# Kernel tuning notes

Hardware: AMD Instinct MI355X
Metric: run time of the kernel (lower is better)

The kernel has to match this reference:

```python
import jax, jax.numpy as jnp
import numpy as np

B, S, H = 2, 4096, 1024
WINDOW = 32


def setup_inputs() -> dict:
    key = jax.random.key(0)
    ks = jax.random.split(key, 10)
    s = 1.0 / np.sqrt(H)
    return {
        "hidden_states": jax.random.normal(ks[0], (B, S, H), dtype=jnp.float32),
        "Wq": jax.random.normal(ks[1], (H, H), dtype=jnp.float32) * s,
        "Wk": jax.random.normal(ks[2], (H, H), dtype=jnp.float32) * s,
        "Wv": jax.random.normal(ks[3], (H, H), dtype=jnp.float32) * s,
        "Wo": jax.random.normal(ks[4], (H, H), dtype=jnp.float32) * s,
        "ln_w": jnp.ones((H,), dtype=jnp.float32),
        "ln_b": jnp.zeros((H,), dtype=jnp.float32),
        "W1": jax.random.normal(ks[5], (H // 2, H), dtype=jnp.float32) * s,
        "b1": jnp.zeros((H // 2,), dtype=jnp.float32),
        "W2": jax.random.normal(ks[6], (H, H // 2), dtype=jnp.float32) * (1.0 / np.sqrt(H // 2)),
        "b2": jnp.zeros((H,), dtype=jnp.float32),
    }


def _layernorm(x, w, b, eps=1e-5):
    mu = jnp.mean(x, axis=-1, keepdims=True)
    var = jnp.var(x, axis=-1, keepdims=True)
    return (x - mu) * jax.lax.rsqrt(var + eps) * w + b


def reference(hidden_states, Wq, Wk, Wv, Wo, ln_w, ln_b, W1, b1, W2, b2):
    x = hidden_states  # [B,S,H]
    q = x @ Wq.T
    k = x @ Wk.T
    v = x @ Wv.T
    # banded causal mask: keep j<=i and j >= i-WINDOW+1
    i = jnp.arange(S)[:, None]
    j = jnp.arange(S)[None, :]
    local_mask = (j <= i) & (j >= i - WINDOW + 1)  # [S,S] bool
    scores = jnp.einsum('bqh,bkh->bqk', q, k) / np.sqrt(H)
    scores = jnp.where(local_mask[None], scores, -jnp.inf)
    probs = jax.nn.softmax(scores, axis=-1)
    attn_out = jnp.einsum('bqk,bkh->bqh', probs, v) @ Wo.T
    draft = x + attn_out
    h = _layernorm(draft, ln_w, ln_b)
    h = jax.nn.gelu(h @ W1.T + b1, approximate=False)
    adapter_out = h @ W2.T + b2
    return draft + adapter_out
```

## Files before the change

### kernel.cpp

```cpp
#include <hip/hip_runtime.h>
#include <stdint.h>

typedef unsigned short u16;
typedef __bf16 bfx8 __attribute__((ext_vector_type(8)));
typedef float f32x4 __attribute__((ext_vector_type(4)));

__device__ __forceinline__ u16 f2bf(float x) {
    unsigned int u = __float_as_uint(x);
    u += 0x7fffu + ((u >> 16) & 1u);
    return (u16)(u >> 16);
}
__device__ __forceinline__ float bf2f(u16 v) {
    return __uint_as_float(((unsigned)v) << 16);
}

__device__ __forceinline__ void async16(const void* g, void* l) {
    __builtin_amdgcn_global_load_lds(
        (const __attribute__((address_space(1))) unsigned int*)(uintptr_t)g,
        (__attribute__((address_space(3))) unsigned int*)(unsigned int)(uintptr_t)l,
        16, 0, 0);
}

#define S_BARRIER() asm volatile("s_barrier" ::: "memory")
#define WAIT_VM6() asm volatile("s_waitcnt vmcnt(6)" ::: "memory")
#define WAIT_VM5() asm volatile("s_waitcnt vmcnt(5)" ::: "memory")
#define WAIT_VM0() asm volatile("s_waitcnt vmcnt(0)" ::: "memory")

struct CastArgs {
    const float* src[7];
    u16* dst[7];
    int nblk[7];
};
__global__ __launch_bounds__(256) void cast_all(CastArgs a) {
    int b = blockIdx.x, seg = 0;
    while (b >= a.nblk[seg]) { b -= a.nblk[seg]; ++seg; }
    int i = b * 256 + threadIdx.x;
    const float4* p = (const float4*)(a.src[seg] + (size_t)i * 8);
    float4 x = p[0], y = p[1];
    ushort4 o0, o1;
    o0.x = f2bf(x.x); o0.y = f2bf(x.y); o0.z = f2bf(x.z); o0.w = f2bf(x.w);
    o1.x = f2bf(y.x); o1.y = f2bf(y.y); o1.z = f2bf(y.z); o1.w = f2bf(y.w);
    ushort4* q = (ushort4*)(a.dst[seg] + (size_t)i * 8);
    q[0] = o0; q[1] = o1;
}

template <int EPI, int BNv>
__global__ __launch_bounds__(512, 2)
void gemm_ring(const u16* __restrict__ A, const u16* __restrict__ Bw,
               u16* __restrict__ outq, u16* __restrict__ outk,
               u16* __restrict__ vt, u16* __restrict__ outb,
               const float* __restrict__ bias, const u16* __restrict__ resb,
               u16* __restrict__ draftb, float* __restrict__ outf,
               int M, int N, int K, int ncol) {
    constexpr int NF = BNv / 32;
    constexpr int BU = BNv / 64;
    constexpr int TS = 32768 + BNv * 128;
    __shared__ __align__(1024) unsigned char lds[3 * TS];
    const int t = threadIdx.x;
    const int lane = t & 63, w = t >> 6;
    const int laneR = lane & 15, laneK = lane >> 4;
    const int wr = w >> 1, wc = w & 1;
    const int b = blockIdx.x;
    const int cpx = gridDim.x >> 3;
    const int swz = (b & 7) * cpx + (b >> 3);
    const int row0 = (swz / ncol) * 256, col0 = (swz % ncol) * BNv;
    const int nt = K >> 6;

    f32x4 acc[4][NF] = {};

    const u16* srcA[4];
    const u16* srcB[BU];
    unsigned dA[4], dB[BU];
#pragma unroll
    for (int i = 0; i < 4; ++i) {
        int li = i * 512 + t;
        int row = li >> 3, ko = li & 7;
        srcA[i] = A + (size_t)(row0 + row) * K + (ko ^ (row & 7)) * 8;
        dA[i] = li * 16;
    }
#pragma unroll
    for (int i = 0; i < BU; ++i) {
        int li = i * 512 + t;
        int row = li >> 3, ko = li & 7;
        srcB[i] = Bw + (size_t)(col0 + row) * K + (ko ^ (row & 7)) * 8;
        dB[i] = 32768 + li * 16;
    }

    auto stage = [&](int rb, int tk, int h) {
        unsigned char* base = lds + rb * TS;
        const int o = tk * 64;
        if (h == 0) {
            async16(srcA[0] + o, base + dA[0]);
            async16(srcA[1] + o, base + dA[1]);
            async16(srcB[0] + o, base + dB[0]);
        } else {
            async16(srcA[2] + o, base + dA[2]);
            async16(srcA[3] + o, base + dA[3]);
            if constexpr (BU == 2) async16(srcB[1] + o, base + dB[1]);
        }
    };

    stage(0, 0, 0); stage(0, 0, 1);
    stage(1, 1, 0); stage(1, 1, 1);

    for (int tk = 0; tk < nt; ++tk) {
        unsigned char* bufA = lds + (tk % 3) * TS;
        unsigned char* bufB = bufA + 32768;
        if (tk + 1 < nt) {
            if constexpr (BU == 2) { WAIT_VM6(); } else { WAIT_VM5(); }
        } else { WAIT_VM0(); }
        S_BARRIER();
        const bool pf = (tk + 2 < nt);
        const int nb = (tk + 2) % 3;
#pragma unroll
        for (int ks = 0; ks < 2; ++ks) {
            bfx8 af[4], bf[NF];
#pragma unroll
            for (int m = 0; m < 4; ++m) {
                int r = wr * 64 + m * 16 + laneR;
                int phys = (ks * 4 + laneK) ^ (r & 7);
                af[m] = *(const bfx8*)(bufA + r * 128 + phys * 16);
            }
#pragma unroll
            for (int n = 0; n < NF; ++n) {
                int r = wc * (BNv / 2) + n * 16 + laneR;
                int phys = (ks * 4 + laneK) ^ (r & 7);
                bf[n] = *(const bfx8*)(bufB + r * 128 + phys * 16);
            }
            if (pf) stage(nb, tk + 2, ks);
            S_BARRIER();
            __builtin_amdgcn_s_setprio(1);
#pragma unroll
            for (int m = 0; m < 4; ++m)
#pragma unroll
                for (int n = 0; n < NF; ++n)
                    acc[m][n] = __builtin_amdgcn_mfma_f32_16x16x32_bf16(
                        af[m], bf[n], acc[m][n], 0, 0, 0);
            __builtin_amdgcn_s_setprio(0);
            S_BARRIER();
        }
    }

#pragma unroll
    for (int m = 0; m < 4; ++m) {
        const int gr0 = row0 + wr * 64 + m * 16 + laneK * 4;
#pragma unroll
        for (int n = 0; n < NF; ++n) {
            const int gc = col0 + wc * (BNv / 2) + n * 16 + laneR;
            if constexpr (EPI == 0) {
                if (col0 < 1024) {
#pragma unroll
                    for (int r = 0; r < 4; ++r)
                        outq[(size_t)(gr0 + r) * 1024 + gc] = f2bf(acc[m][n][r]);
                } else if (col0 < 2048) {
#pragma unroll
                    for (int r = 0; r < 4; ++r)
                        outk[(size_t)(gr0 + r) * 1024 + (gc - 1024)] = f2bf(acc[m][n][r]);
                } else {
                    ushort4 o4;
                    o4.x = f2bf(acc[m][n][0]); o4.y = f2bf(acc[m][n][1]);
                    o4.z = f2bf(acc[m][n][2]); o4.w = f2bf(acc[m][n][3]);
                    *(ushort4*)(vt + (((size_t)(gr0 >> 12)) * 1024 + (gc - 2048)) * 4096 +
                                (gr0 & 4095)) = o4;
                }
            } else if constexpr (EPI == 1) {
#pragma unroll
                for (int r = 0; r < 4; ++r) {
                    size_t idx = (size_t)(gr0 + r) * N + gc;
                    draftb[idx] = f2bf(bf2f(resb[idx]) + acc[m][n][r]);
                }
            } else if constexpr (EPI == 2) {
#pragma unroll
                for (int r = 0; r < 4; ++r) {
                    float xx = acc[m][n][r] + bias[gc];
                    outb[(size_t)(gr0 + r) * N + gc] =
                        f2bf(xx * 0.5f * (1.0f + erff(xx * 0.70710678118654752f)));
                }
            } else {
#pragma unroll
                for (int r = 0; r < 4; ++r) {
                    size_t idx = (size_t)(gr0 + r) * N + gc;
                    outf[idx] = bf2f(draftb[idx]) + acc[m][n][r] + bias[gc];
                }
            }
        }
    }
}

__global__ __launch_bounds__(256, 2)
void attn_kernel(const u16* __restrict__ Q, const u16* __restrict__ K,
                 const u16* __restrict__ vt, u16* __restrict__ O) {
    constexpr int H = 1024, S = 4096;
    const int t = threadIdx.x, lane = t & 63, w = t >> 6;
    const int laneR = lane & 15, laneK = lane >> 4;
    const int bb = blockIdx.x;
    const int tile = (bb & 7) * 32 + (bb >> 3);
    const int batch = tile >> 7;
    const int i0 = (tile & 127) * 32;
    const size_t base = (size_t)batch * S * H;

    __shared__ __align__(16) float S4[4][32][64];
    __shared__ __align__(16) u16 P[32][72];

    f32x4 sc[2][4] = {};
    for (int h = w * 256; h < w * 256 + 256; h += 32) {
        bfx8 qa[2];
#pragma unroll
        for (int m = 0; m < 2; ++m) {
            size_t row = (size_t)(i0 + m * 16 + laneR);
            qa[m] = *(const bfx8*)(Q + base + row * H + h + laneK * 8);
        }
        bfx8 kb[4];
#pragma unroll
        for (int n = 0; n < 4; ++n) {
            int j = i0 - 32 + n * 16 + laneR;
            int jc = j < 0 ? 0 : j;
            kb[n] = *(const bfx8*)(K + base + (size_t)jc * H + h + laneK * 8);
        }
#pragma unroll
        for (int m = 0; m < 2; ++m)
#pragma unroll
            for (int n = 0; n < 4; ++n)
                sc[m][n] = __builtin_amdgcn_mfma_f32_16x16x32_bf16(
                    qa[m], kb[n], sc[m][n], 0, 0, 0);
    }
#pragma unroll
    for (int m = 0; m < 2; ++m)
#pragma unroll
        for (int n = 0; n < 4; ++n)
#pragma unroll
            for (int r = 0; r < 4; ++r)
                S4[w][m * 16 + laneK * 4 + r][n * 16 + laneR] = sc[m][n][r];
    __syncthreads();

    {
        int q = t >> 3;
        int c0 = (t & 7) * 8;
        int lo = q + 1;
        if (32 - i0 > lo) lo = 32 - i0;
        int hi = q + 32;
        float vals[8];
        float mx = -1e30f;
#pragma unroll
        for (int c = 0; c < 8; ++c) {
            int cc = c0 + c;
            float v = (S4[0][q][cc] + S4[1][q][cc] + S4[2][q][cc] + S4[3][q][cc]) * 0.03125f;
            bool valid = (cc >= lo) && (cc <= hi);
            vals[c] = valid ? v : -1e30f;
            if (vals[c] > mx) mx = vals[c];
        }
#pragma unroll
        for (int d = 1; d < 8; d <<= 1) {
            float o = __shfl_xor(mx, d);
            if (o > mx) mx = o;
        }
        float sum = 0.f;
        float es[8];
#pragma unroll
        for (int c = 0; c < 8; ++c) {
            es[c] = (vals[c] > -1e29f) ? __expf(vals[c] - mx) : 0.f;
            sum += es[c];
        }
#pragma unroll
        for (int d = 1; d < 8; d <<= 1) sum += __shfl_xor(sum, d);
        float inv = 1.0f / sum;
#pragma unroll
        for (int c = 0; c < 8; ++c) P[q][c0 + c] = f2bf(es[c] * inv);
    }
    __syncthreads();

    for (int nc = 0; nc < 4; ++nc) {
        int ncol = w * 256 + nc * 64;
        f32x4 o[2][4] = {};
#pragma unroll
        for (int ks = 0; ks < 2; ++ks) {
            bfx8 pa[2];
#pragma unroll
            for (int m = 0; m < 2; ++m)
                pa[m] = *(const bfx8*)(&P[m * 16 + laneR][ks * 32 + laneK * 8]);
            int t0 = i0 - 32 + ks * 32 + laneK * 8;
            if (t0 < 0) t0 = 0;
#pragma unroll
            for (int n = 0; n < 4; ++n) {
                int c = ncol + n * 16 + laneR;
                bfx8 vb = *(const bfx8*)(vt + ((size_t)batch * 1024 + c) * 4096 + t0);
#pragma unroll
                for (int m = 0; m < 2; ++m)
                    o[m][n] = __builtin_amdgcn_mfma_f32_16x16x32_bf16(
                        pa[m], vb, o[m][n], 0, 0, 0);
            }
        }
#pragma unroll
        for (int m = 0; m < 2; ++m)
#pragma unroll
            for (int n = 0; n < 4; ++n)
#pragma unroll
                for (int r = 0; r < 4; ++r) {
                    size_t row = (size_t)(i0 + m * 16 + laneK * 4 + r);
                    O[base + row * H + ncol + n * 16 + laneR] = f2bf(o[m][n][r]);
                }
    }
}

__global__ __launch_bounds__(256)
void ln_kernel(const u16* __restrict__ xb, const float* __restrict__ gw,
               const float* __restrict__ gb, u16* __restrict__ out) {
    const int row = blockIdx.x, t = threadIdx.x;
    const ushort4 dv = ((const ushort4*)(xb + (size_t)row * 1024))[t];
    float4 v;
    v.x = bf2f(dv.x); v.y = bf2f(dv.y); v.z = bf2f(dv.z); v.w = bf2f(dv.w);
    float s = v.x + v.y + v.z + v.w;
    float s2 = v.x * v.x + v.y * v.y + v.z * v.z + v.w * v.w;
#pragma unroll
    for (int d = 1; d < 64; d <<= 1) {
        s += __shfl_xor(s, d);
        s2 += __shfl_xor(s2, d);
    }
    __shared__ float red[8];
    int lane = t & 63, wv = t >> 6;
    if (lane == 0) { red[wv] = s; red[4 + wv] = s2; }
    __syncthreads();
    float S1 = red[0] + red[1] + red[2] + red[3];
    float S2 = red[4] + red[5] + red[6] + red[7];
    float mu = S1 * (1.0f / 1024.0f);
    float var = S2 * (1.0f / 1024.0f) - mu * mu;
    float rstd = rsqrtf(var + 1e-5f);
    const float4 wv4 = ((const float4*)gw)[t];
    const float4 bv4 = ((const float4*)gb)[t];
    ushort4 o;
    o.x = f2bf((v.x - mu) * rstd * wv4.x + bv4.x);
    o.y = f2bf((v.y - mu) * rstd * wv4.y + bv4.y);
    o.z = f2bf((v.z - mu) * rstd * wv4.z + bv4.z);
    o.w = f2bf((v.w - mu) * rstd * wv4.w + bv4.w);
    ((ushort4*)(out + (size_t)row * 1024))[t] = o;
}

extern "C" void kernel_launch(void* const* d_in, const int* in_sizes, int n_in,
                              void* d_out, int out_size, void* d_ws, size_t ws_size,
                              hipStream_t stream) {
    const float* x   = (const float*)d_in[0];
    const float* Wq  = (const float*)d_in[1];
    const float* Wk  = (const float*)d_in[2];
    const float* Wv  = (const float*)d_in[3];
    const float* Wo  = (const float*)d_in[4];
    const float* lnw = (const float*)d_in[5];
    const float* lnb = (const float*)d_in[6];
    const float* W1  = (const float*)d_in[7];
    const float* b1  = (const float*)d_in[8];
    const float* W2  = (const float*)d_in[9];
    const float* b2  = (const float*)d_in[10];
    (void)in_sizes; (void)n_in; (void)out_size; (void)ws_size;

    const int M = 8192, H = 1024, Hh = 512;

    char* ws = (char*)d_ws;
    size_t off = 0;
    auto alloc = [&](size_t bytes) {
        char* p = ws + off;
        off += (bytes + 255) & ~(size_t)255;
        return p;
    };
    u16* Xb     = (u16*)alloc((size_t)M * H * 2);
    u16* Wqkvb  = (u16*)alloc((size_t)3 * H * H * 2);
    u16* Wob    = (u16*)alloc((size_t)H * H * 2);
    u16* W1b    = (u16*)alloc((size_t)Hh * H * 2);
    u16* W2b    = (u16*)alloc((size_t)H * Hh * 2);
    u16* Qb     = (u16*)alloc((size_t)M * H * 2);
    u16* Kb     = (u16*)alloc((size_t)M * H * 2);
    u16* Vt     = (u16*)alloc((size_t)M * H * 2);
    u16* draftb = (u16*)alloc((size_t)M * H * 2);
    u16* Attb   = (u16*)alloc((size_t)M * H * 2);
    u16* hlnb = Qb;
    u16* Gb   = Kb;
    float* outp = (float*)d_out;

    CastArgs ca;
    ca.src[0] = x;  ca.dst[0] = Xb;                        ca.nblk[0] = (M * H / 8) / 256;
    ca.src[1] = Wq; ca.dst[1] = Wqkvb;                     ca.nblk[1] = (H * H / 8) / 256;
    ca.src[2] = Wk; ca.dst[2] = Wqkvb + (size_t)H * H;     ca.nblk[2] = (H * H / 8) / 256;
    ca.src[3] = Wv; ca.dst[3] = Wqkvb + (size_t)2 * H * H; ca.nblk[3] = (H * H / 8) / 256;
    ca.src[4] = Wo; ca.dst[4] = Wob;                       ca.nblk[4] = (H * H / 8) / 256;
    ca.src[5] = W1; ca.dst[5] = W1b;                       ca.nblk[5] = (Hh * H / 8) / 256;
    ca.src[6] = W2; ca.dst[6] = W2b;                       ca.nblk[6] = (H * Hh / 8) / 256;
    int totblk = 0;
    for (int i = 0; i < 7; ++i) totblk += ca.nblk[i];
    cast_all<<<dim3(totblk), dim3(256), 0, stream>>>(ca);

    gemm_ring<0, 128><<<dim3(768), dim3(512), 0, stream>>>(
        Xb, Wqkvb, Qb, Kb, Vt, nullptr, nullptr, nullptr, nullptr, nullptr,
        M, 3 * H, H, 24);

    attn_kernel<<<dim3(256), dim3(256), 0, stream>>>(Qb, Kb, Vt, Attb);

    gemm_ring<1, 128><<<dim3(256), dim3(512), 0, stream>>>(
        Attb, Wob, nullptr, nullptr, nullptr, nullptr, nullptr, Xb, draftb, nullptr,
        M, H, H, 8);

    ln_kernel<<<dim3(M), dim3(256), 0, stream>>>(draftb, lnw, lnb, hlnb);

    gemm_ring<2, 64><<<dim3(256), dim3(512), 0, stream>>>(
        hlnb, W1b, nullptr, nullptr, nullptr, Gb, b1, nullptr, nullptr, nullptr,
        M, Hh, H, 8);

    gemm_ring<3, 128><<<dim3(256), dim3(512), 0, stream>>>(
        Gb, W2b, nullptr, nullptr, nullptr, nullptr, b2, nullptr, draftb, outp,
        M, H, Hh, 8);
}
```

Before: 168.8 us.

## Add dedicated 256x256-tile QKV GEMM with double-buffered staged loads

Replaces the generic 256x128 ring GEMM for the fused QKV projection with a specialised kernel using 256x256 tiles, a 2x4 wave layout and 128 KB double-buffered LDS. Loads for the next k-tile are interleaved in quarter-chunks between MFMA phases. This is meant to raise operand reuse and cut global traffic per FLOP. The generic GEMM also moves its vmcnt wait and barrier to the end of each iteration so the wait overlaps the tail of the MFMA phase. Risks include lower occupancy from the large LDS footprint, more barriers per iteration, and fewer blocks (384) to fill the GPU.

New measurement: 167.9 us. Within noise of the previous version (-0.5%).

```diff
diff --git a/kernel.cpp b/kernel.cpp
--- a/kernel.cpp
+++ b/kernel.cpp
@@ -24,6 +24,7 @@
 #define S_BARRIER() asm volatile("s_barrier" ::: "memory")
 #define WAIT_VM6() asm volatile("s_waitcnt vmcnt(6)" ::: "memory")
 #define WAIT_VM5() asm volatile("s_waitcnt vmcnt(5)" ::: "memory")
+#define WAIT_VM2() asm volatile("s_waitcnt vmcnt(2)" ::: "memory")
 #define WAIT_VM0() asm volatile("s_waitcnt vmcnt(0)" ::: "memory")
 
 struct CastArgs {
@@ -44,14 +45,149 @@
     q[0] = o0; q[1] = o1;
 }
 
+__global__ __launch_bounds__(512, 2)
+void gemm_qkv2(const u16* __restrict__ A, const u16* __restrict__ Bw,
+               u16* __restrict__ outq, u16* __restrict__ outk,
+               u16* __restrict__ vt, int K) {
+    __shared__ __align__(1024) unsigned char lds[131072];
+    const int t = threadIdx.x;
+    const int lane = t & 63, w = t >> 6;
+    const int laneR = lane & 15, laneK = lane >> 4;
+    const int wm = w >> 2, wn = w & 3;
+    const int b = blockIdx.x;
+    const int swz = (b & 7) * 48 + (b >> 3);
+    const int row0 = (swz / 12) * 256;
+    const int col0 = (swz % 12) * 256;
+    const int nt = K >> 6;
+
+    const u16* srcU[4][2];
+    unsigned dstU[4][2];
+#pragma unroll
+    for (int u = 0; u < 4; ++u)
+#pragma unroll
+        for (int j = 0; j < 2; ++j) {
+            int c = ((u & 1) ? 1024 : 0) + j * 512 + t;
+            int row = c >> 3;
+            int ko = (c & 7) ^ (row & 7);
+            if (u < 2) srcU[u][j] = A + (size_t)(row0 + row) * K + ko * 8;
+            else       srcU[u][j] = Bw + (size_t)(col0 + row) * K + ko * 8;
+            dstU[u][j] = (u >= 2 ? 32768u : 0u) + (unsigned)c * 16u;
+        }
+
+#define QSTAGE(U, D, TK)                                                      \
+    async16(srcU[U][0] + (TK) * 64, lds + (D) + dstU[U][0]);                  \
+    async16(srcU[U][1] + (TK) * 64, lds + (D) + dstU[U][1]);
+
+    f32x4 acc[8][4] = {};
+    bfx8 af[4], bf[4];
+
+#define QLDA(D, KS, H)                                                        \
+    _Pragma("unroll") for (int m = 0; m < 4; ++m) {                           \
+        int r = (H) * 128 + wm * 64 + m * 16 + laneR;                         \
+        int ph = ((KS) * 4 + laneK) ^ (r & 7);                                \
+        af[m] = *(const bfx8*)(lds + (D) + r * 128 + ph * 16);                \
+    }
+#define QLDB(D, KS)                                                           \
+    _Pragma("unroll") for (int n = 0; n < 4; ++n) {                           \
+        int rb = wn * 64 + n * 16 + laneR;                                    \
+        int ph = ((KS) * 4 + laneK) ^ (rb & 7);                               \
+        bf[n] = *(const bfx8*)(lds + (D) + 32768u + rb * 128 + ph * 16);      \
+    }
+#define QMFMA(H)                                                              \
+    __builtin_amdgcn_s_setprio(1);                                            \
+    _Pragma("unroll") for (int m = 0; m < 4; ++m)                             \
+        _Pragma("unroll") for (int n = 0; n < 4; ++n)                         \
+            acc[(H) * 4 + m][n] = __builtin_amdgcn_mfma_f32_16x16x32_bf16(    \
+                af[m], bf[n], acc[(H) * 4 + m][n], 0, 0, 0);                  \
+    __builtin_amdgcn_s_setprio(0);
+
+    QSTAGE(0, 0u, 0) QSTAGE(2, 0u, 0) QSTAGE(3, 0u, 0) QSTAGE(1, 0u, 0)
+    WAIT_VM2();
+    S_BARRIER();
+
+    for (int tk = 0; tk < nt - 1; ++tk) {
+        const unsigned d = (unsigned)(tk & 1) * 65536u;
+        const unsigned nd = d ^ 65536u;
+        const int tn = tk + 1;
+        QLDA(d, 0, 0) QLDB(d, 0) QSTAGE(0, nd, tn)
+        S_BARRIER();
+        QMFMA(0)
+        WAIT_VM2();
+        S_BARRIER();
+        QLDA(d, 0, 1) QSTAGE(2, nd, tn)
+        S_BARRIER();
+        QMFMA(1)
+        S_BARRIER();
+        QLDA(d, 1, 0) QLDB(d, 1) QSTAGE(3, nd, tn)
+        S_BARRIER();
+        QMFMA(0)
+        S_BARRIER();
+        QLDA(d, 1, 1) QSTAGE(1, nd, tn)
+        S_BARRIER();
+        QMFMA(1)
+        WAIT_VM2();
+        S_BARRIER();
+    }
+    {
+        const unsigned d = (unsigned)((nt - 1) & 1) * 65536u;
+        QLDA(d, 0, 0) QLDB(d, 0)
+        S_BARRIER();
+        QMFMA(0)
+        WAIT_VM0();
+        S_BARRIER();
+        QLDA(d, 0, 1)
+        S_BARRIER();
+        QMFMA(1)
+        S_BARRIER();
+        QLDA(d, 1, 0) QLDB(d, 1)
+        S_BARRIER();
+        QMFMA(0)
+        S_BARRIER();
+        QLDA(d, 1, 1)
+        S_BARRIER();
+        QMFMA(1)
+    }
+
+    const int colsec = col0 >> 10;
+#pragma unroll
+    for (int hi = 0; hi < 2; ++hi) {
+#pragma unroll
+        for (int mi = 0; mi < 4; ++mi) {
+            const int gr0 = row0 + hi * 128 + wm * 64 + mi * 16 + laneK * 4;
+#pragma unroll
+            for (int n = 0; n < 4; ++n) {
+                const int gc = col0 + wn * 64 + n * 16 + laneR;
+                const f32x4 a4 = acc[hi * 4 + mi][n];
+                if (colsec == 0) {
+#pragma unroll
+                    for (int r = 0; r < 4; ++r)
+                        outq[(size_t)(gr0 + r) * 1024 + gc] = f2bf(a4[r]);
+                } else if (colsec == 1) {
+#pragma unroll
+                    for (int r = 0; r < 4; ++r)
+                        outk[(size_t)(gr0 + r) * 1024 + (gc - 1024)] = f2bf(a4[r]);
+                } else {
+                    ushort4 o4;
+                    o4.x = f2bf(a4[0]); o4.y = f2bf(a4[1]);
+                    o4.z = f2bf(a4[2]); o4.w = f2bf(a4[3]);
+                    *(ushort4*)(vt + (((size_t)(gr0 >> 12)) * 1024 + (gc - 2048)) * 4096 +
+                                (gr0 & 4095)) = o4;
+                }
+            }
+        }
+    }
+#undef QSTAGE
+#undef QLDA
+#undef QLDB
+#undef QMFMA
+}
+
 template <int EPI, int BNv>
 __global__ __launch_bounds__(512, 2)
 void gemm_ring(const u16* __restrict__ A, const u16* __restrict__ Bw,
-               u16* __restrict__ outq, u16* __restrict__ outk,
-               u16* __restrict__ vt, u16* __restrict__ outb,
-               const float* __restrict__ bias, const u16* __restrict__ resb,
-               u16* __restrict__ draftb, float* __restrict__ outf,
-               int M, int N, int K, int ncol) {
+               u16* __restrict__ outb, const float* __restrict__ bias,
+               const u16* __restrict__ resb, u16* __restrict__ draftb,
+               float* __restrict__ outf, int M, int N, int K, int ncol) {
     constexpr int NF = BNv / 32;
     constexpr int BU = BNv / 64;
     constexpr int TS = 32768 + BNv * 128;
@@ -102,14 +238,12 @@
 
     stage(0, 0, 0); stage(0, 0, 1);
     stage(1, 1, 0); stage(1, 1, 1);
+    if constexpr (BU == 2) { WAIT_VM6(); } else { WAIT_VM5(); }
+    S_BARRIER();
 
     for (int tk = 0; tk < nt; ++tk) {
         unsigned char* bufA = lds + (tk % 3) * TS;
         unsigned char* bufB = bufA + 32768;
-        if (tk + 1 < nt) {
-            if constexpr (BU == 2) { WAIT_VM6(); } else { WAIT_VM5(); }
-        } else { WAIT_VM0(); }
-        S_BARRIER();
         const bool pf = (tk + 2 < nt);
         const int nb = (tk + 2) % 3;
 #pragma unroll
@@ -137,6 +271,13 @@
                     acc[m][n] = __builtin_amdgcn_mfma_f32_16x16x32_bf16(
                         af[m], bf[n], acc[m][n], 0, 0, 0);
             __builtin_amdgcn_s_setprio(0);
+            if (ks == 1) {
+                if (pf) {
+                    if constexpr (BU == 2) { WAIT_VM6(); } else { WAIT_VM5(); }
+                } else {
+                    WAIT_VM0();
+                }
+            }
             S_BARRIER();
         }
     }
@@ -147,23 +288,7 @@
 #pragma unroll
         for (int n = 0; n < NF; ++n) {
             const int gc = col0 + wc * (BNv / 2) + n * 16 + laneR;
-            if constexpr (EPI == 0) {
-                if (col0 < 1024) {
-#pragma unroll
-                    for (int r = 0; r < 4; ++r)
-                        outq[(size_t)(gr0 + r) * 1024 + gc] = f2bf(acc[m][n][r]);
-                } else if (col0 < 2048) {
-#pragma unroll
-                    for (int r = 0; r < 4; ++r)
-                        outk[(size_t)(gr0 + r) * 1024 + (gc - 1024)] = f2bf(acc[m][n][r]);
-                } else {
-                    ushort4 o4;
-                    o4.x = f2bf(acc[m][n][0]); o4.y = f2bf(acc[m][n][1]);
-                    o4.z = f2bf(acc[m][n][2]); o4.w = f2bf(acc[m][n][3]);
-                    *(ushort4*)(vt + (((size_t)(gr0 >> 12)) * 1024 + (gc - 2048)) * 4096 +
-                                (gr0 & 4095)) = o4;
-                }
-            } else if constexpr (EPI == 1) {
+            if constexpr (EPI == 1) {
 #pragma unroll
                 for (int r = 0; r < 4; ++r) {
                     size_t idx = (size_t)(gr0 + r) * N + gc;
@@ -386,23 +511,18 @@
     for (int i = 0; i < 7; ++i) totblk += ca.nblk[i];
     cast_all<<<dim3(totblk), dim3(256), 0, stream>>>(ca);
 
-    gemm_ring<0, 128><<<dim3(768), dim3(512), 0, stream>>>(
-        Xb, Wqkvb, Qb, Kb, Vt, nullptr, nullptr, nullptr, nullptr, nullptr,
-        M, 3 * H, H, 24);
+    gemm_qkv2<<<dim3(384), dim3(512), 0, stream>>>(Xb, Wqkvb, Qb, Kb, Vt, H);
 
     attn_kernel<<<dim3(256), dim3(256), 0, stream>>>(Qb, Kb, Vt, Attb);
 
     gemm_ring<1, 128><<<dim3(256), dim3(512), 0, stream>>>(
-        Attb, Wob, nullptr, nullptr, nullptr, nullptr, nullptr, Xb, draftb, nullptr,
-        M, H, H, 8);
+        Attb, Wob, nullptr, nullptr, Xb, draftb, nullptr, M, H, H, 8);
 
     ln_kernel<<<dim3(M), dim3(256), 0, stream>>>(draftb, lnw, lnb, hlnb);
 
     gemm_ring<2, 64><<<dim3(256), dim3(512), 0, stream>>>(
-        hlnb, W1b, nullptr, nullptr, nullptr, Gb, b1, nullptr, nullptr, nullptr,
-        M, Hh, H, 8);
+        hlnb, W1b, Gb, b1, nullptr, nullptr, nullptr, M, Hh, H, 8);
 
     gemm_ring<3, 128><<<dim3(256), dim3(512), 0, stream>>>(
-        Gb, W2b, nullptr, nullptr, nullptr, nullptr, b2, nullptr, draftb, outp,
-        M, H, Hh, 8);
-}
+        Gb, W2b, nullptr, b2, nullptr, draftb, outp, M, H, Hh, 8);
+}
```

## Use simple single-buffer 128x128 QKV GEMM and move ring-buffer wait to loop end

Applied to the files above, without the earlier changes.

Replaces the QKV projection, which used the 256x128 triple-buffered ring GEMM, with a new 128x128-tile, 256-thread kernel that loads each K-slice directly into one LDS buffer between syncthreads and can hold four blocks per CU. The grid doubles to 1536 blocks, giving more blocks to spread across CUs at the cost of no intra-block prefetch overlap. Separately, the ring GEMM moves its vmcnt wait and barrier from the top of each iteration to the end of the second k-substep, so the wait sits after the MFMAs. The QKV epilogue is removed from the ring template and its argument list is trimmed.

Result: faster. 164.4 us, median of 3 (-2.6%).

```diff
diff --git a/kernel.cpp b/kernel.cpp
--- a/kernel.cpp
+++ b/kernel.cpp
@@ -44,14 +44,101 @@
     q[0] = o0; q[1] = o1;
 }
 
+__global__ __launch_bounds__(256, 4)
+void gemm97_qkv(const u16* __restrict__ A, const u16* __restrict__ Bw,
+                u16* __restrict__ outq, u16* __restrict__ outk,
+                u16* __restrict__ vt, int K, int ncol) {
+    __shared__ __align__(1024) unsigned char lds[32768];
+    const int t = threadIdx.x;
+    const int lane = t & 63, w = t >> 6;
+    const int laneR = lane & 15, laneK = lane >> 4;
+    const int wr = w >> 1, wc = w & 1;
+    const int b = blockIdx.x;
+    const int cpx = gridDim.x >> 3;
+    const int swz = (b & 7) * cpx + (b >> 3);
+    const int row0 = (swz / ncol) * 128, col0 = (swz % ncol) * 128;
+    const int nt = K >> 6;
+
+    f32x4 acc[4][4] = {};
+
+    const u16* srcA[4];
+    const u16* srcB[4];
+    unsigned dA[4], dB[4];
+#pragma unroll
+    for (int i = 0; i < 4; ++i) {
+        int li = i * 256 + t;
+        int row = li >> 3, ko = li & 7;
+        int kos = (ko ^ (row & 7)) * 8;
+        srcA[i] = A + (size_t)(row0 + row) * K + kos;
+        srcB[i] = Bw + (size_t)(col0 + row) * K + kos;
+        dA[i] = li * 16;
+        dB[i] = 16384 + li * 16;
+    }
+
+    for (int tk = 0; tk < nt; ++tk) {
+        const int o = tk * 64;
+#pragma unroll
+        for (int i = 0; i < 4; ++i) {
+            async16(srcA[i] + o, lds + dA[i]);
+            async16(srcB[i] + o, lds + dB[i]);
+        }
+        __syncthreads();
+#pragma unroll
+        for (int ks = 0; ks < 2; ++ks) {
+            bfx8 af[4], bf[4];
+#pragma unroll
+            for (int m = 0; m < 4; ++m) {
+                int r = wr * 64 + m * 16 + laneR;
+                int ph = (ks * 4 + laneK) ^ (r & 7);
+                af[m] = *(const bfx8*)(lds + r * 128 + ph * 16);
+            }
+#pragma unroll
+            for (int n = 0; n < 4; ++n) {
+                int r = wc * 64 + n * 16 + laneR;
+                int ph = (ks * 4 + laneK) ^ (r & 7);
+                bf[n] = *(const bfx8*)(lds + 16384 + r * 128 + ph * 16);
+            }
+#pragma unroll
+            for (int m = 0; m < 4; ++m)
+#pragma unroll
+                for (int n = 0; n < 4; ++n)
+                    acc[m][n] = __builtin_amdgcn_mfma_f32_16x16x32_bf16(
+                        af[m], bf[n], acc[m][n], 0, 0, 0);
+        }
+        __syncthreads();
+    }
+
+#pragma unroll
+    for (int m = 0; m < 4; ++m) {
+        const int gr0 = row0 + wr * 64 + m * 16 + laneK * 4;
+#pragma unroll
+        for (int n = 0; n < 4; ++n) {
+            const int gc = col0 + wc * 64 + n * 16 + laneR;
+            if (col0 < 1024) {
+#pragma unroll
+                for (int r = 0; r < 4; ++r)
+                    outq[(size_t)(gr0 + r) * 1024 + gc] = f2bf(acc[m][n][r]);
+            } else if (col0 < 2048) {
+#pragma unroll
+                for (int r = 0; r < 4; ++r)
+                    outk[(size_t)(gr0 + r) * 1024 + (gc - 1024)] = f2bf(acc[m][n][r]);
+            } else {
+                ushort4 o4;
+                o4.x = f2bf(acc[m][n][0]); o4.y = f2bf(acc[m][n][1]);
+                o4.z = f2bf(acc[m][n][2]); o4.w = f2bf(acc[m][n][3]);
+                *(ushort4*)(vt + (((size_t)(gr0 >> 12)) * 1024 + (gc - 2048)) * 4096 +
+                            (gr0 & 4095)) = o4;
+            }
+        }
+    }
+}
+
 template <int EPI, int BNv>
 __global__ __launch_bounds__(512, 2)
 void gemm_ring(const u16* __restrict__ A, const u16* __restrict__ Bw,
-               u16* __restrict__ outq, u16* __restrict__ outk,
-               u16* __restrict__ vt, u16* __restrict__ outb,
-               const float* __restrict__ bias, const u16* __restrict__ resb,
-               u16* __restrict__ draftb, float* __restrict__ outf,
-               int M, int N, int K, int ncol) {
+               u16* __restrict__ outb, const float* __restrict__ bias,
+               const u16* __restrict__ resb, u16* __restrict__ draftb,
+               float* __restrict__ outf, int M, int N, int K, int ncol) {
     constexpr int NF = BNv / 32;
     constexpr int BU = BNv / 64;
     constexpr int TS = 32768 + BNv * 128;
@@ -102,14 +189,12 @@
 
     stage(0, 0, 0); stage(0, 0, 1);
     stage(1, 1, 0); stage(1, 1, 1);
+    if constexpr (BU == 2) { WAIT_VM6(); } else { WAIT_VM5(); }
+    S_BARRIER();
 
     for (int tk = 0; tk < nt; ++tk) {
         unsigned char* bufA = lds + (tk % 3) * TS;
         unsigned char* bufB = bufA + 32768;
-        if (tk + 1 < nt) {
-            if constexpr (BU == 2) { WAIT_VM6(); } else { WAIT_VM5(); }
-        } else { WAIT_VM0(); }
-        S_BARRIER();
         const bool pf = (tk + 2 < nt);
         const int nb = (tk + 2) % 3;
 #pragma unroll
@@ -137,6 +222,13 @@
                     acc[m][n] = __builtin_amdgcn_mfma_f32_16x16x32_bf16(
                         af[m], bf[n], acc[m][n], 0, 0, 0);
             __builtin_amdgcn_s_setprio(0);
+            if (ks == 1) {
+                if (pf) {
+                    if constexpr (BU == 2) { WAIT_VM6(); } else { WAIT_VM5(); }
+                } else {
+                    WAIT_VM0();
+                }
+            }
             S_BARRIER();
         }
     }
@@ -147,23 +239,7 @@
 #pragma unroll
         for (int n = 0; n < NF; ++n) {
             const int gc = col0 + wc * (BNv / 2) + n * 16 + laneR;
-            if constexpr (EPI == 0) {
-                if (col0 < 1024) {
-#pragma unroll
-                    for (int r = 0; r < 4; ++r)
-                        outq[(size_t)(gr0 + r) * 1024 + gc] = f2bf(acc[m][n][r]);
-                } else if (col0 < 2048) {
-#pragma unroll
-                    for (int r = 0; r < 4; ++r)
-                        outk[(size_t)(gr0 + r) * 1024 + (gc - 1024)] = f2bf(acc[m][n][r]);
-                } else {
-                    ushort4 o4;
-                    o4.x = f2bf(acc[m][n][0]); o4.y = f2bf(acc[m][n][1]);
-                    o4.z = f2bf(acc[m][n][2]); o4.w = f2bf(acc[m][n][3]);
-                    *(ushort4*)(vt + (((size_t)(gr0 >> 12)) * 1024 + (gc - 2048)) * 4096 +
-                                (gr0 & 4095)) = o4;
-                }
-            } else if constexpr (EPI == 1) {
+            if constexpr (EPI == 1) {
 #pragma unroll
                 for (int r = 0; r < 4; ++r) {
                     size_t idx = (size_t)(gr0 + r) * N + gc;
@@ -386,23 +462,19 @@
     for (int i = 0; i < 7; ++i) totblk += ca.nblk[i];
     cast_all<<<dim3(totblk), dim3(256), 0, stream>>>(ca);
 
-    gemm_ring<0, 128><<<dim3(768), dim3(512), 0, stream>>>(
-        Xb, Wqkvb, Qb, Kb, Vt, nullptr, nullptr, nullptr, nullptr, nullptr,
-        M, 3 * H, H, 24);
+    gemm97_qkv<<<dim3(1536), dim3(256), 0, stream>>>(
+        Xb, Wqkvb, Qb, Kb, Vt, H, 24);
 
     attn_kernel<<<dim3(256), dim3(256), 0, stream>>>(Qb, Kb, Vt, Attb);
 
     gemm_ring<1, 128><<<dim3(256), dim3(512), 0, stream>>>(
-        Attb, Wob, nullptr, nullptr, nullptr, nullptr, nullptr, Xb, draftb, nullptr,
-        M, H, H, 8);
+        Attb, Wob, nullptr, nullptr, Xb, draftb, nullptr, M, H, H, 8);
 
     ln_kernel<<<dim3(M), dim3(256), 0, stream>>>(draftb, lnw, lnb, hlnb);
 
     gemm_ring<2, 64><<<dim3(256), dim3(512), 0, stream>>>(
-        hlnb, W1b, nullptr, nullptr, nullptr, Gb, b1, nullptr, nullptr, nullptr,
-        M, Hh, H, 8);
+        hlnb, W1b, Gb, b1, nullptr, nullptr, nullptr, M, Hh, H, 8);
 
     gemm_ring<3, 128><<<dim3(256), dim3(512), 0, stream>>>(
-        Gb, W2b, nullptr, nullptr, nullptr, nullptr, b2, nullptr, draftb, outp,
-        M, H, Hh, 8);
-}
+        Gb, W2b, nullptr, b2, nullptr, draftb, outp, M, H, Hh, 8);
+}
```
